# Kernel optimization log

Hardware: AMD Instinct MI355X
Metric: run time of the kernel (lower is better)

Reference implementation:

```python
import jax, jax.numpy as jnp
import numpy as np

EPS = 1e-12  # torch F.normalize eps


def _l2norm(x):
    n = jnp.linalg.norm(x, axis=-1, keepdims=True)
    return x / jnp.maximum(n, EPS)


def setup_inputs() -> dict:
    key = jax.random.key(0)
    k1, k2 = jax.random.split(key)
    B, Lq, Lk, D = 128, 32, 128, 128
    left_emb = jax.random.normal(k1, (B, Lq, D), dtype=jnp.float32)
    right_emb = jax.random.normal(k2, (B, Lk, D), dtype=jnp.float32)
    pos_idx = jnp.arange(B, dtype=jnp.int64)
    logit_scale = jnp.asarray(np.log(1.0 / 0.07), dtype=jnp.float32)  # scalar param
    return {"left_emb": left_emb, "right_emb": right_emb,
            "logit_scale": logit_scale, "pos_idx": pos_idx}


def reference(left_emb, right_emb, logit_scale, pos_idx):
    # maxsim_colbert: normalize token embeddings, cross-sim, max over doc
    # tokens, sum over query tokens -> [B, B] logits, then CE loss.
    l = _l2norm(left_emb)   # [B, Lq, D]
    r = _l2norm(right_emb)  # [B, Lk, D]
    sims = jnp.einsum('xik,yjk->xyij', l, r)        # [B, B, Lq, Lk]
    sim = sims.max(axis=-1).sum(axis=-1)            # [B, B]
    logits = jnp.exp(logit_scale) * sim
    logp = jax.nn.log_softmax(logits, axis=1)
    B = logits.shape[0]
    loss = -jnp.mean(logp[jnp.arange(B), pos_idx])
    return loss
```

## Files before the change

kernel.cpp:

```cpp
#include <hip/hip_runtime.h>
#include <hip/hip_bf16.h>

typedef short bf16x8 __attribute__((ext_vector_type(8)));
typedef float f32x16 __attribute__((ext_vector_type(16)));
typedef unsigned short u16;

#define B 128
#define LQ 32
#define LK 128
#define D 128
#define YPB 4


static __device__ inline u16 f2bf_rne(float f) {
  union { float f; unsigned u; } v; v.f = f;
  unsigned r = v.u + 0x7fffu + ((v.u >> 16) & 1u);
  return (u16)(r >> 16);
}

__global__ __launch_bounds__(256) void normalize_kernel(
    const float* __restrict__ left, const float* __restrict__ right,
    char* __restrict__ lbf, char* __restrict__ rbf) {
  int wave = (blockIdx.x * blockDim.x + threadIdx.x) >> 6;
  int lane = threadIdx.x & 63;
  const int n_l = B * LQ;
  const float* src; char* dst;
  if (wave < n_l) {
    int x = wave >> 5, i = wave & 31;
    src = left + (size_t)wave * D;
    dst = lbf + x * 8192 + i * 16;
  } else {
    int row = wave - n_l;
    int y = row >> 7, j = row & 127;
    src = right + (size_t)row * D;
    dst = rbf + y * 32768 + (j >> 5) * 8192 + (j & 31) * 16;
  }
  float2 v = *reinterpret_cast<const float2*>(src + lane * 2);
  float ss = v.x * v.x + v.y * v.y;
#pragma unroll
  for (int off = 1; off < 64; off <<= 1) ss += __shfl_xor(ss, off);
  float inv = 1.0f / fmaxf(sqrtf(ss), 1e-12f);
  unsigned packed = (unsigned)f2bf_rne(v.x * inv) |
                    ((unsigned)f2bf_rne(v.y * inv) << 16);
  *reinterpret_cast<unsigned*>(
      dst + (lane >> 3) * 1024 + ((lane >> 2) & 1) * 512 + (lane & 3) * 4) = packed;
}

__global__ __launch_bounds__(256, 2) void maxsim_kernel(
    const char* __restrict__ lbf, const char* __restrict__ rbf,
    float* __restrict__ sims) {
  const int lane = threadIdx.x & 63;
  const int wv   = threadIdx.x >> 6;
  const int xg   = blockIdx.x >> 5;
  const int yg   = blockIdx.x & 31;
  const int x0   = xg * 8 + wv * 2;
  const int lane16 = lane * 16;

  bf16x8 bfr[2][8];
#pragma unroll
  for (int xi = 0; xi < 2; ++xi)
#pragma unroll
    for (int ks = 0; ks < 8; ++ks)
      bfr[xi][ks] = *reinterpret_cast<const bf16x8*>(
          lbf + (x0 + xi) * 8192 + ks * 1024 + lane16);

  f32x16 z;
#pragma unroll
  for (int t = 0; t < 16; ++t) z[t] = 0.f;

  const char* rb0 = rbf + (size_t)(yg * YPB) * 32768;

#define LOADA(dst, s_next)                                                   \
  {                                                                          \
    const char* nb = rb0 + ((s_next) >> 2) * 32768 + ((s_next) & 3) * 8192;  \
    _Pragma("unroll")                                                        \
    for (int ks = 0; ks < 8; ++ks)                                           \
      dst[ks] = *reinterpret_cast<const bf16x8*>(nb + ks * 1024 + lane16);   \
  }

#define MFMAB(srcA)                                                          \
  __builtin_amdgcn_s_setprio(1);                                             \
  a0 = __builtin_amdgcn_mfma_f32_32x32x16_bf16(srcA[0], bfr[0][0], z, 0, 0, 0); \
  a1 = __builtin_amdgcn_mfma_f32_32x32x16_bf16(srcA[0], bfr[1][0], z, 0, 0, 0); \
  _Pragma("unroll")                                                          \
  for (int ks = 1; ks < 8; ++ks) {                                           \
    a0 = __builtin_amdgcn_mfma_f32_32x32x16_bf16(srcA[ks], bfr[0][ks], a0, 0, 0, 0); \
    a1 = __builtin_amdgcn_mfma_f32_32x32x16_bf16(srcA[ks], bfr[1][ks], a1, 0, 0, 0); \
  }                                                                          \
  __builtin_amdgcn_s_setprio(0);

  bf16x8 pA[8], pB[8];
  LOADA(pA, 0);

#pragma unroll
  for (int yy = 0; yy < YPB; ++yy) {
    float cm0 = -3.0e38f, cm1 = -3.0e38f;
#pragma unroll
    for (int mj = 0; mj < 4; ++mj) {
      const int s = yy * 4 + mj;
      f32x16 a0, a1;
      if ((s & 1) == 0) {
        if (s < 15) LOADA(pB, s + 1);
        MFMAB(pA);
      } else {
        if (s < 15) LOADA(pA, s + 1);
        MFMAB(pB);
      }
#pragma unroll
      for (int t = 0; t < 16; t += 4) {
        cm0 = fmaxf(cm0, fmaxf(fmaxf(a0[t], a0[t + 1]), fmaxf(a0[t + 2], a0[t + 3])));
        cm1 = fmaxf(cm1, fmaxf(fmaxf(a1[t], a1[t + 1]), fmaxf(a1[t + 2], a1[t + 3])));
      }
    }
    cm0 = fmaxf(cm0, __shfl_xor(cm0, 32));
    cm1 = fmaxf(cm1, __shfl_xor(cm1, 32));
#pragma unroll
    for (int off = 1; off <= 16; off <<= 1) {
      cm0 += __shfl_xor(cm0, off);
      cm1 += __shfl_xor(cm1, off);
    }
    if (lane == 0) {
      const int y = yg * YPB + yy;
      sims[(x0 + 0) * B + y] = cm0;
      sims[(x0 + 1) * B + y] = cm1;
    }
  }
#undef LOADA
#undef MFMAB
}

__global__ __launch_bounds__(1024) void loss_kernel(
    const float* __restrict__ sims, const float* __restrict__ logit_scale,
    const int* __restrict__ pos_idx, float* __restrict__ out) {
  __shared__ float red[16];
  const int lane = threadIdx.x & 63;
  const int wv   = threadIdx.x >> 6;
  const float scale = expf(logit_scale[0]);
  float local = 0.f;
#pragma unroll
  for (int rr = 0; rr < 8; ++rr) {
    const int x = wv * 8 + rr;
    const float* row = sims + x * B;
    float a = row[lane], b2 = row[64 + lane];
    float m = fmaxf(a, b2);
#pragma unroll
    for (int off = 1; off < 64; off <<= 1) m = fmaxf(m, __shfl_xor(m, off));
    float ml = scale * m;
    float e = expf(scale * a - ml) + expf(scale * b2 - ml);
#pragma unroll
    for (int off = 1; off < 64; off <<= 1) e += __shfl_xor(e, off);
    int pos = pos_idx[x];
    float pv = __shfl(pos < 64 ? a : b2, pos & 63);
    local += -(scale * pv - ml - logf(e));
  }
  if (lane == 0) red[wv] = local;
  __syncthreads();
  if (threadIdx.x == 0) {
    float t = 0.f;
#pragma unroll
    for (int i = 0; i < 16; ++i) t += red[i];
    out[0] = t / (float)B;
  }
}

extern "C" void kernel_launch(void* const* d_in, const int* in_sizes, int n_in,
                              void* d_out, int out_size, void* d_ws, size_t ws_size,
                              hipStream_t stream) {
  const float* left  = (const float*)d_in[0];
  const float* right = (const float*)d_in[1];
  const float* ls    = (const float*)d_in[2];
  const int*   pos   = (const int*)d_in[3];
  float* out = (float*)d_out;

  char* ws  = (char*)d_ws;
  char* lbf = ws;
  char* rbf = ws + (size_t)B * LQ * D * 2;
  float* sims = (float*)(ws + (size_t)B * LQ * D * 2 + (size_t)B * LK * D * 2);

  int waves = B * LQ + B * LK;
  normalize_kernel<<<waves / 4, 256, 0, stream>>>(left, right, lbf, rbf);
  maxsim_kernel<<<512, 256, 0, stream>>>(lbf, rbf, sims);
  loss_kernel<<<1, 1024, 0, stream>>>(sims, ls, pos, out);
}
```

Measured before the change: 35.78 us.

## Give each wave one query instead of two and remap blocks for XCD locality

```diff
diff --git a/kernel.cpp b/kernel.cpp
--- a/kernel.cpp
+++ b/kernel.cpp
@@ -9,7 +9,6 @@
 #define LQ 32
 #define LK 128
 #define D 128
-#define YPB 4
 
 
 static __device__ inline u16 f2bf_rne(float f) {
@@ -26,14 +25,12 @@
   const int n_l = B * LQ;
   const float* src; char* dst;
   if (wave < n_l) {
-    int x = wave >> 5, i = wave & 31;
     src = left + (size_t)wave * D;
-    dst = lbf + x * 8192 + i * 16;
+    dst = lbf + (wave >> 5) * 8192 + (wave & 31) * 16;
   } else {
     int row = wave - n_l;
-    int y = row >> 7, j = row & 127;
     src = right + (size_t)row * D;
-    dst = rbf + y * 32768 + (j >> 5) * 8192 + (j & 31) * 16;
+    dst = rbf + (row >> 7) * 32768 + ((row >> 5) & 3) * 8192 + (row & 31) * 16;
   }
   float2 v = *reinterpret_cast<const float2*>(src + lane * 2);
   float ss = v.x * v.x + v.y * v.y;
@@ -46,87 +43,74 @@
       dst + (lane >> 3) * 1024 + ((lane >> 2) & 1) * 512 + (lane & 3) * 4) = packed;
 }
 
-__global__ __launch_bounds__(256, 2) void maxsim_kernel(
+__global__ __launch_bounds__(256, 4) void maxsim_kernel(
     const char* __restrict__ lbf, const char* __restrict__ rbf,
     float* __restrict__ sims) {
   const int lane = threadIdx.x & 63;
   const int wv   = threadIdx.x >> 6;
-  const int xg   = blockIdx.x >> 5;
-  const int yg   = blockIdx.x & 31;
-  const int x0   = xg * 8 + wv * 2;
+  const int bid  = blockIdx.x;
+  const int xcd  = bid & 7;
+  const int w    = bid >> 3;
+  const int yg   = xcd * 4 + (w & 3);
+  const int xg   = w >> 2;
+  const int x    = xg * 4 + wv;
   const int lane16 = lane * 16;
 
-  bf16x8 bfr[2][8];
+  bf16x8 bfr[8];
 #pragma unroll
-  for (int xi = 0; xi < 2; ++xi)
-#pragma unroll
-    for (int ks = 0; ks < 8; ++ks)
-      bfr[xi][ks] = *reinterpret_cast<const bf16x8*>(
-          lbf + (x0 + xi) * 8192 + ks * 1024 + lane16);
+  for (int ks = 0; ks < 8; ++ks)
+    bfr[ks] = *reinterpret_cast<const bf16x8*>(
+        lbf + x * 8192 + ks * 1024 + lane16);
 
-  f32x16 z;
-#pragma unroll
-  for (int t = 0; t < 16; ++t) z[t] = 0.f;
-
-  const char* rb0 = rbf + (size_t)(yg * YPB) * 32768;
+  const char* rb0 = rbf + (size_t)yg * 4 * 32768;
 
 #define LOADA(dst, s_next)                                                   \
   {                                                                          \
-    const char* nb = rb0 + ((s_next) >> 2) * 32768 + ((s_next) & 3) * 8192;  \
+    const char* nb = rb0 + (s_next) * 8192;                                  \
     _Pragma("unroll")                                                        \
     for (int ks = 0; ks < 8; ++ks)                                           \
       dst[ks] = *reinterpret_cast<const bf16x8*>(nb + ks * 1024 + lane16);   \
   }
 
-#define MFMAB(srcA)                                                          \
+#define MFMA8(srcA)                                                          \
   __builtin_amdgcn_s_setprio(1);                                             \
-  a0 = __builtin_amdgcn_mfma_f32_32x32x16_bf16(srcA[0], bfr[0][0], z, 0, 0, 0); \
-  a1 = __builtin_amdgcn_mfma_f32_32x32x16_bf16(srcA[0], bfr[1][0], z, 0, 0, 0); \
   _Pragma("unroll")                                                          \
-  for (int ks = 1; ks < 8; ++ks) {                                           \
-    a0 = __builtin_amdgcn_mfma_f32_32x32x16_bf16(srcA[ks], bfr[0][ks], a0, 0, 0, 0); \
-    a1 = __builtin_amdgcn_mfma_f32_32x32x16_bf16(srcA[ks], bfr[1][ks], a1, 0, 0, 0); \
-  }                                                                          \
+  for (int t = 0; t < 16; ++t) acc[t] = 0.f;                                 \
+  _Pragma("unroll")                                                          \
+  for (int ks = 0; ks < 8; ++ks)                                             \
+    acc = __builtin_amdgcn_mfma_f32_32x32x16_bf16(srcA[ks], bfr[ks], acc,    \
+                                                  0, 0, 0);                  \
   __builtin_amdgcn_s_setprio(0);
 
   bf16x8 pA[8], pB[8];
+  f32x16 acc;
   LOADA(pA, 0);
 
 #pragma unroll
-  for (int yy = 0; yy < YPB; ++yy) {
-    float cm0 = -3.0e38f, cm1 = -3.0e38f;
+  for (int yy = 0; yy < 4; ++yy) {
+    float cm = -3.0e38f;
 #pragma unroll
     for (int mj = 0; mj < 4; ++mj) {
       const int s = yy * 4 + mj;
-      f32x16 a0, a1;
       if ((s & 1) == 0) {
         if (s < 15) LOADA(pB, s + 1);
-        MFMAB(pA);
+        MFMA8(pA);
       } else {
         if (s < 15) LOADA(pA, s + 1);
-        MFMAB(pB);
+        MFMA8(pB);
       }
 #pragma unroll
-      for (int t = 0; t < 16; t += 4) {
-        cm0 = fmaxf(cm0, fmaxf(fmaxf(a0[t], a0[t + 1]), fmaxf(a0[t + 2], a0[t + 3])));
-        cm1 = fmaxf(cm1, fmaxf(fmaxf(a1[t], a1[t + 1]), fmaxf(a1[t + 2], a1[t + 3])));
-      }
+      for (int t = 0; t < 16; t += 4)
+        cm = fmaxf(cm, fmaxf(fmaxf(acc[t], acc[t + 1]),
+                             fmaxf(acc[t + 2], acc[t + 3])));
     }
-    cm0 = fmaxf(cm0, __shfl_xor(cm0, 32));
-    cm1 = fmaxf(cm1, __shfl_xor(cm1, 32));
+    cm = fmaxf(cm, __shfl_xor(cm, 32));
 #pragma unroll
-    for (int off = 1; off <= 16; off <<= 1) {
-      cm0 += __shfl_xor(cm0, off);
-      cm1 += __shfl_xor(cm1, off);
-    }
-    if (lane == 0) {
-      const int y = yg * YPB + yy;
-      sims[(x0 + 0) * B + y] = cm0;
-      sims[(x0 + 1) * B + y] = cm1;
-    }
+    for (int off = 1; off <= 16; off <<= 1) cm += __shfl_xor(cm, off);
+    if (lane == 0) sims[x * B + (yg * 4 + yy)] = cm;
   }
 #undef LOADA
-#undef MFMAB
+#undef MFMA8
 }
 
 __global__ __launch_bounds__(1024) void loss_kernel(
@@ -174,11 +158,11 @@
 
   char* ws  = (char*)d_ws;
   char* lbf = ws;
-  char* rbf = ws + (size_t)B * LQ * D * 2;
-  float* sims = (float*)(ws + (size_t)B * LQ * D * 2 + (size_t)B * LK * D * 2);
+  char* rbf = ws + (size_t)(1 << 20);
+  float* sims = (float*)(ws + (size_t)(5 << 20));
 
   int waves = B * LQ + B * LK;
   normalize_kernel<<<waves / 4, 256, 0, stream>>>(left, right, lbf, rbf);
-  maxsim_kernel<<<512, 256, 0, stream>>>(lbf, rbf, sims);
+  maxsim_kernel<<<1024, 256, 0, stream>>>(lbf, rbf, sims);
   loss_kernel<<<1, 1024, 0, stream>>>(sims, ls, pos, out);
 }
```

Result: slower. 39.12 us (+9.3%).
